# Optimization experiments

Hardware: AMD Instinct MI355X
Metric: run time of the kernel (lower is better)

## Reference

```python
import jax, jax.numpy as jnp
import numpy as np

NUM_GRAPHS = 128
HIDDEN = 256
EPS = 1e-8


def setup_inputs() -> dict:
    key = jax.random.key(0)
    k1, k2, k3, k4, k5, k6, k7 = jax.random.split(key, 7)
    N = 100000
    node_feat = jax.random.normal(k1, (N, HIDDEN), dtype=jnp.float32)
    node_pos = jax.random.normal(k2, (N, 3), dtype=jnp.float32)
    batch = jnp.sort(jax.random.randint(k3, (N,), 0, NUM_GRAPHS))
    # mlp_node_feat: Linear(1, hidden) -> SiLU -> Linear(hidden, hidden)
    W1 = jax.random.normal(k4, (1, HIDDEN), dtype=jnp.float32) * (1.0 / np.sqrt(1.0))
    b1 = jax.random.normal(k5, (HIDDEN,), dtype=jnp.float32) * 0.01
    W2 = jax.random.normal(k6, (HIDDEN, HIDDEN), dtype=jnp.float32) * (1.0 / np.sqrt(HIDDEN))
    b2 = jax.random.normal(k7, (HIDDEN,), dtype=jnp.float32) * 0.01
    return {"node_feat": node_feat, "node_pos": node_pos, "batch": batch,
            "W1": W1, "b1": b1, "W2": W2, "b2": b2}


def _scatter_mean(x, seg, num_segments):
    # sum per segment / count (empty segments -> 0, matching nan_to_num)
    sums = jax.ops.segment_sum(x, seg, num_segments=num_segments)
    counts = jax.ops.segment_sum(jnp.ones((x.shape[0], 1), x.dtype), seg,
                                 num_segments=num_segments)
    return jnp.where(counts > 0, sums / jnp.maximum(counts, 1.0), 0.0)


def reference(node_feat, node_pos, batch, W1, b1, W2, b2):
    # center of each graph, gathered back to nodes
    center = _scatter_mean(node_pos, batch, NUM_GRAPHS)          # [G, 3]
    pos = node_pos - center[batch]                               # [N, 3]
    # safe_norm with keepdim
    scalar = jnp.maximum(jnp.linalg.norm(pos, axis=1, keepdims=True), EPS)  # [N, 1]
    # mlp_node_feat: Linear -> SiLU -> Linear
    h = jax.nn.silu(scalar @ W1 + b1)                            # [N, H]
    return h @ W2 + b2                                           # [N, H]
```

## Files before the change

### kernel.cpp

```cpp
#include <hip/hip_runtime.h>
#include <math.h>

#define HIDDEN   256
#define G_NUM    128
#define TN       1024
#define DS       (1.0f/64.0f)
#define INV_DS   64.0f
#define TM       4
#define TBLOCKS  (TN/TM)
#define LGRID    2048

typedef float f32x4 __attribute__((ext_vector_type(4)));

__device__ __forceinline__ float readlane_f(float v, int l) {
    union { float f; unsigned u; } a, r;
    a.f = v;
    r.u = __builtin_amdgcn_readlane(a.u, l);
    return r.f;
}

__device__ __forceinline__ float silu_f(float x) {
    return x / (1.f + __expf(-x));
}

__global__ __launch_bounds__(256)
void prep_kernel(const float* __restrict__ pos,
                 const int*   __restrict__ batch,
                 const float* __restrict__ W1,
                 const float* __restrict__ b1,
                 const float* __restrict__ W2,
                 const float* __restrict__ b2,
                 int N,
                 float* __restrict__ center,
                 float* __restrict__ T)
{
    const int bid = blockIdx.x;
    const int tid = threadIdx.x;

    if (bid < TBLOCKS) {
        int k  = tid;
        int l  = tid & 63;
        int m0 = bid * TM;
        float s0 = (float)(m0 + 0) * DS;
        float s1 = (float)(m0 + 1) * DS;
        float s2 = (float)(m0 + 2) * DS;
        float s3 = (float)(m0 + 3) * DS;
        float a0 = 0.f, a1 = 0.f, a2 = 0.f, a3 = 0.f;

        for (int c = 0; c < HIDDEN / 64; ++c) {
            int jb = c * 64;
            float w1 = W1[jb + l];
            float bb = b1[jb + l];
            float h0 = silu_f(fmaf(s0, w1, bb));
            float h1 = silu_f(fmaf(s1, w1, bb));
            float h2 = silu_f(fmaf(s2, w1, bb));
            float h3 = silu_f(fmaf(s3, w1, bb));
            const float* w2p = W2 + (size_t)jb * HIDDEN + k;
            #pragma unroll
            for (int jj = 0; jj < 64; ++jj) {
                float w = w2p[(size_t)jj * HIDDEN];
                a0 = fmaf(readlane_f(h0, jj), w, a0);
                a1 = fmaf(readlane_f(h1, jj), w, a1);
                a2 = fmaf(readlane_f(h2, jj), w, a2);
                a3 = fmaf(readlane_f(h3, jj), w, a3);
            }
        }
        float bv = b2[k];
        T[(size_t)(m0 + 0) * HIDDEN + k] = a0 + bv;
        T[(size_t)(m0 + 1) * HIDDEN + k] = a1 + bv;
        T[(size_t)(m0 + 2) * HIDDEN + k] = a2 + bv;
        T[(size_t)(m0 + 3) * HIDDEN + k] = a3 + bv;
        return;
    }

    const int g = bid - TBLOCKS;

    int lo0 = 0, hi0 = N, lo1 = 0, hi1 = N;
    while (lo0 < hi0 || lo1 < hi1) {
        if (lo0 < hi0) { int m = (lo0 + hi0) >> 1; if (batch[m] <  g) lo0 = m + 1; else hi0 = m; }
        if (lo1 < hi1) { int m = (lo1 + hi1) >> 1; if (batch[m] <= g) lo1 = m + 1; else hi1 = m; }
    }
    const int start = lo0, end = lo1;
    const int cnt = end - start;
    if (cnt <= 0) {
        if (tid == 0) {
            center[g * 4 + 0] = 0.f; center[g * 4 + 1] = 0.f; center[g * 4 + 2] = 0.f;
        }
        return;
    }

    float sx = 0.f, sy = 0.f, sz = 0.f;
    for (int n = start + tid; n < end; n += 256) {
        sx += pos[n * 3 + 0];
        sy += pos[n * 3 + 1];
        sz += pos[n * 3 + 2];
    }
    #pragma unroll
    for (int m = 32; m > 0; m >>= 1) {
        sx += __shfl_xor(sx, m, 64);
        sy += __shfl_xor(sy, m, 64);
        sz += __shfl_xor(sz, m, 64);
    }
    __shared__ float cw[3][4];
    const int w    = tid >> 6;
    const int lane = tid & 63;
    if (lane == 0) { cw[0][w] = sx; cw[1][w] = sy; cw[2][w] = sz; }
    __syncthreads();
    if (tid == 0) {
        float inv = 1.f / (float)cnt;
        center[g * 4 + 0] = (cw[0][0] + cw[0][1] + cw[0][2] + cw[0][3]) * inv;
        center[g * 4 + 1] = (cw[1][0] + cw[1][1] + cw[1][2] + cw[1][3]) * inv;
        center[g * 4 + 2] = (cw[2][0] + cw[2][1] + cw[2][2] + cw[2][3]) * inv;
    }
}

__global__ __launch_bounds__(256)
void lerp_kernel(const float* __restrict__ pos,
                 const int*   __restrict__ batch,
                 const float* __restrict__ center,
                 const float* __restrict__ T,
                 float* __restrict__ out, int N)
{
    const int w      = (blockIdx.x << 2) | (threadIdx.x >> 6);
    const int l      = threadIdx.x & 63;
    const int stride = LGRID * 4;

    const f32x4* T4   = (const f32x4*)T;
    f32x4*       out4 = (f32x4*)out;

    int n = w;
    for (; n + 2 * stride < N; n += 3 * stride) {
        int n1 = n + stride;
        int n2 = n1 + stride;
        int   g0 = batch[n],  g1 = batch[n1], g2 = batch[n2];
        float x0 = pos[n  * 3 + 0], y0 = pos[n  * 3 + 1], z0 = pos[n  * 3 + 2];
        float x1 = pos[n1 * 3 + 0], y1 = pos[n1 * 3 + 1], z1 = pos[n1 * 3 + 2];
        float x2 = pos[n2 * 3 + 0], y2 = pos[n2 * 3 + 1], z2 = pos[n2 * 3 + 2];
        float dx0 = x0 - center[g0 * 4 + 0], dy0 = y0 - center[g0 * 4 + 1], dz0 = z0 - center[g0 * 4 + 2];
        float dx1 = x1 - center[g1 * 4 + 0], dy1 = y1 - center[g1 * 4 + 1], dz1 = z1 - center[g1 * 4 + 2];
        float dx2 = x2 - center[g2 * 4 + 0], dy2 = y2 - center[g2 * 4 + 1], dz2 = z2 - center[g2 * 4 + 2];
        float u0 = fmaxf(sqrtf(fmaf(dx0, dx0, fmaf(dy0, dy0, dz0 * dz0))), 1e-8f) * INV_DS;
        float u1 = fmaxf(sqrtf(fmaf(dx1, dx1, fmaf(dy1, dy1, dz1 * dz1))), 1e-8f) * INV_DS;
        float u2 = fmaxf(sqrtf(fmaf(dx2, dx2, fmaf(dy2, dy2, dz2 * dz2))), 1e-8f) * INV_DS;
        int   i0 = (int)u0; i0 = (i0 < TN - 2) ? i0 : (TN - 2);
        int   i1 = (int)u1; i1 = (i1 < TN - 2) ? i1 : (TN - 2);
        int   i2 = (int)u2; i2 = (i2 < TN - 2) ? i2 : (TN - 2);
        float f0 = u0 - (float)i0;
        float f1 = u1 - (float)i1;
        float f2 = u2 - (float)i2;
        f32x4 A0 = T4[(size_t)i0       * (HIDDEN / 4) + l];
        f32x4 B0 = T4[(size_t)(i0 + 1) * (HIDDEN / 4) + l];
        f32x4 A1 = T4[(size_t)i1       * (HIDDEN / 4) + l];
        f32x4 B1 = T4[(size_t)(i1 + 1) * (HIDDEN / 4) + l];
        f32x4 A2 = T4[(size_t)i2       * (HIDDEN / 4) + l];
        f32x4 B2 = T4[(size_t)(i2 + 1) * (HIDDEN / 4) + l];
        f32x4 o0, o1, o2;
        o0.x = fmaf(f0, B0.x - A0.x, A0.x);
        o0.y = fmaf(f0, B0.y - A0.y, A0.y);
        o0.z = fmaf(f0, B0.z - A0.z, A0.z);
        o0.w = fmaf(f0, B0.w - A0.w, A0.w);
        o1.x = fmaf(f1, B1.x - A1.x, A1.x);
        o1.y = fmaf(f1, B1.y - A1.y, A1.y);
        o1.z = fmaf(f1, B1.z - A1.z, A1.z);
        o1.w = fmaf(f1, B1.w - A1.w, A1.w);
        o2.x = fmaf(f2, B2.x - A2.x, A2.x);
        o2.y = fmaf(f2, B2.y - A2.y, A2.y);
        o2.z = fmaf(f2, B2.z - A2.z, A2.z);
        o2.w = fmaf(f2, B2.w - A2.w, A2.w);
        __builtin_nontemporal_store(o0, &out4[(size_t)n  * (HIDDEN / 4) + l]);
        __builtin_nontemporal_store(o1, &out4[(size_t)n1 * (HIDDEN / 4) + l]);
        __builtin_nontemporal_store(o2, &out4[(size_t)n2 * (HIDDEN / 4) + l]);
    }
    for (; n < N; n += stride) {
        int   g0 = batch[n];
        float x0 = pos[n * 3 + 0], y0 = pos[n * 3 + 1], z0 = pos[n * 3 + 2];
        float dx0 = x0 - center[g0 * 4 + 0], dy0 = y0 - center[g0 * 4 + 1], dz0 = z0 - center[g0 * 4 + 2];
        float u0 = fmaxf(sqrtf(fmaf(dx0, dx0, fmaf(dy0, dy0, dz0 * dz0))), 1e-8f) * INV_DS;
        int   i0 = (int)u0; i0 = (i0 < TN - 2) ? i0 : (TN - 2);
        float f0 = u0 - (float)i0;
        f32x4 A0 = T4[(size_t)i0       * (HIDDEN / 4) + l];
        f32x4 B0 = T4[(size_t)(i0 + 1) * (HIDDEN / 4) + l];
        f32x4 o0;
        o0.x = fmaf(f0, B0.x - A0.x, A0.x);
        o0.y = fmaf(f0, B0.y - A0.y, A0.y);
        o0.z = fmaf(f0, B0.z - A0.z, A0.z);
        o0.w = fmaf(f0, B0.w - A0.w, A0.w);
        __builtin_nontemporal_store(o0, &out4[(size_t)n * (HIDDEN / 4) + l]);
    }
}

extern "C" void kernel_launch(void* const* d_in, const int* in_sizes, int n_in,
                              void* d_out, int out_size, void* d_ws, size_t ws_size,
                              hipStream_t stream) {
    const float* node_pos = (const float*)d_in[1];
    const int*   batch    = (const int*)  d_in[2];
    const float* W1       = (const float*)d_in[3];
    const float* b1       = (const float*)d_in[4];
    const float* W2       = (const float*)d_in[5];
    const float* b2       = (const float*)d_in[6];
    float*       out      = (float*)d_out;

    int N = in_sizes[1] / 3;

    char*  ws     = (char*)d_ws;
    float* center = (float*)ws;
    float* T      = (float*)(ws + 4096);

    prep_kernel<<<TBLOCKS + G_NUM, 256, 0, stream>>>(node_pos, batch,
                                                     W1, b1, W2, b2, N,
                                                     center, T);
    lerp_kernel<<<LGRID, 256, 0, stream>>>(node_pos, batch, center, T, out, N);
}
```

Measured before the change: 32.72 us.

## Replace per-graph binary search with parallel boundary detection kernel

```diff
diff --git a/kernel.cpp b/kernel.cpp
--- a/kernel.cpp
+++ b/kernel.cpp
@@ -24,15 +24,14 @@
 }
 
 __global__ __launch_bounds__(256)
-void prep_kernel(const float* __restrict__ pos,
-                 const int*   __restrict__ batch,
-                 const float* __restrict__ W1,
-                 const float* __restrict__ b1,
-                 const float* __restrict__ W2,
-                 const float* __restrict__ b2,
-                 int N,
-                 float* __restrict__ center,
-                 float* __restrict__ T)
+void table_bounds_kernel(const float* __restrict__ W1,
+                         const float* __restrict__ b1,
+                         const float* __restrict__ W2,
+                         const float* __restrict__ b2,
+                         const int*   __restrict__ batch,
+                         int N,
+                         int* __restrict__ bnd0, int* __restrict__ bnd1,
+                         float* __restrict__ T)
 {
     const int bid = blockIdx.x;
     const int tid = threadIdx.x;
@@ -70,18 +69,34 @@
         T[(size_t)(m0 + 1) * HIDDEN + k] = a1 + bv;
         T[(size_t)(m0 + 2) * HIDDEN + k] = a2 + bv;
         T[(size_t)(m0 + 3) * HIDDEN + k] = a3 + bv;
-        return;
-    }
-
-    const int g = bid - TBLOCKS;
-
-    int lo0 = 0, hi0 = N, lo1 = 0, hi1 = N;
-    while (lo0 < hi0 || lo1 < hi1) {
-        if (lo0 < hi0) { int m = (lo0 + hi0) >> 1; if (batch[m] <  g) lo0 = m + 1; else hi0 = m; }
-        if (lo1 < hi1) { int m = (lo1 + hi1) >> 1; if (batch[m] <= g) lo1 = m + 1; else hi1 = m; }
-    }
-    const int start = lo0, end = lo1;
-    const int cnt = end - start;
+    } else {
+        int n = (bid - TBLOCKS) * 256 + tid;
+        if (n < N) {
+            int bn = batch[n];
+            int bp = (n == 0) ? -1 : batch[n - 1];
+            if (bn != bp) {
+                for (int g = bp + 1; g <= bn; ++g) bnd0[g] = n;
+                for (int g = (bp < 0 ? 0 : bp); g < bn; ++g) bnd1[g] = n;
+            }
+            if (n == N - 1) {
+                for (int g = bn; g < G_NUM; ++g) bnd1[g] = N;
+                for (int g = bn + 1; g < G_NUM; ++g) bnd0[g] = N;
+            }
+        }
+    }
+}
+
+__global__ __launch_bounds__(256)
+void center_kernel(const float* __restrict__ pos,
+                   const int*   __restrict__ bnd0,
+                   const int*   __restrict__ bnd1,
+                   float* __restrict__ center)
+{
+    const int g   = blockIdx.x;
+    const int tid = threadIdx.x;
+    const int start = bnd0[g];
+    const int end   = bnd1[g];
+    const int cnt   = end - start;
     if (cnt <= 0) {
         if (tid == 0) {
             center[g * 4 + 0] = 0.f; center[g * 4 + 1] = 0.f; center[g * 4 + 2] = 0.f;
@@ -203,11 +218,16 @@
     int N = in_sizes[1] / 3;
 
     char*  ws     = (char*)d_ws;
-    float* center = (float*)ws;
+    int*   bnd0   = (int*)ws;
+    int*   bnd1   = (int*)(ws + 512);
+    float* center = (float*)(ws + 1024);
     float* T      = (float*)(ws + 4096);
 
-    prep_kernel<<<TBLOCKS + G_NUM, 256, 0, stream>>>(node_pos, batch,
-                                                     W1, b1, W2, b2, N,
-                                                     center, T);
+    int boundsBlocks = (N + 255) / 256;
+    table_bounds_kernel<<<TBLOCKS + boundsBlocks, 256, 0, stream>>>(
+        W1, b1, W2, b2, batch, N, bnd0, bnd1, T);
+
+    center_kernel<<<G_NUM, 256, 0, stream>>>(node_pos, bnd0, bnd1, center);
+
     lerp_kernel<<<LGRID, 256, 0, stream>>>(node_pos, batch, center, T, out, N);
 }
```

Result: slower. 35.40 us (+8.2%).
